# Kernel tuning notes

Measured on AMD Instinct MI355X. Metric: run time of the kernel, lower is better.

## Reference

```python
import jax, jax.numpy as jnp
import numpy as np

B, T = 32, 1024
TEMP_IN, STAT_IN = 128, 64
TEMP_OUT, STAT_OUT = 128, 64
EPS = 1e-5
NEG_SLOPE = 0.01


def _bn_eval(x, gamma, beta, mean, var):
    # BatchNorm1d in eval mode (running stats)
    return (x - mean) * jax.lax.rsqrt(var + EPS) * gamma + beta


def _leaky_relu(x):
    return jnp.where(x >= 0, x, NEG_SLOPE * x)


def setup_inputs() -> dict:
    key = jax.random.key(0)
    k = jax.random.split(key, 6)
    # deterministic ragged lengths in [512, 1024]
    lengths_np = (512 + (np.arange(B) * 37) % 513).astype(np.int64)
    N = int(lengths_np.sum())  # 23450
    batch_idx = np.repeat(np.arange(B), lengths_np).astype(np.int32)
    pos_idx = np.concatenate([np.arange(l) for l in lengths_np]).astype(np.int32)
    valid = (np.arange(T)[None, :] < lengths_np[:, None])  # [B, T]
    mask_repeat = valid[:, :, None] & valid[:, None, :]    # [B, T, T]

    inp = {
        "x_temp": jax.random.normal(k[0], (N, TEMP_IN), jnp.float32),
        "x_stat": jax.random.normal(k[1], (B, STAT_IN), jnp.float32),
        "temp_attn": jax.random.normal(k[2], (B, T, T), jnp.float32) * 0.1,
        "mask_repeat": jnp.asarray(mask_repeat),
        "lengths": jnp.asarray(lengths_np),
        "batch_idx": jnp.asarray(batch_idx),
        "pos_idx": jnp.asarray(pos_idx),
        # non_linear_temp: Linear(TEMP_IN+STAT_IN -> TEMP_OUT) + BN
        "W1": jax.random.normal(k[3], (TEMP_OUT, TEMP_IN + STAT_IN), jnp.float32) / np.sqrt(TEMP_IN + STAT_IN),
        "b1": jnp.zeros((TEMP_OUT,), jnp.float32),
        "gamma1": jnp.ones((TEMP_OUT,), jnp.float32),
        "beta1": jnp.zeros((TEMP_OUT,), jnp.float32),
        "mean1": jnp.zeros((TEMP_OUT,), jnp.float32),
        "var1": jnp.ones((TEMP_OUT,), jnp.float32),
        # non_linear_stat: Linear(STAT_IN -> STAT_OUT) + BN
        "W2": jax.random.normal(k[4], (STAT_OUT, STAT_IN), jnp.float32) / np.sqrt(STAT_IN),
        "b2": jnp.zeros((STAT_OUT,), jnp.float32),
        "gamma2": jnp.ones((STAT_OUT,), jnp.float32),
        "beta2": jnp.zeros((STAT_OUT,), jnp.float32),
        "mean2": jnp.zeros((STAT_OUT,), jnp.float32),
        "var2": jnp.ones((STAT_OUT,), jnp.float32),
    }
    return inp


def reference(x_temp, x_stat, temp_attn, mask_repeat, lengths, batch_idx, pos_idx,
              W1, b1, gamma1, beta1, mean1, var1,
              W2, b2, gamma2, beta2, mean2, var2):
    # repeat_static_features: gather per-batch static feats to packed rows
    x_stat_rep = x_stat[batch_idx]                              # [N, STAT_IN]
    h = jnp.concatenate((x_temp, x_stat_rep), axis=-1) @ W1.T + b1
    h = _leaky_relu(_bn_eval(h, gamma1, beta1, mean1, var1))    # [N, TEMP_OUT]

    # pad_packed_sequences: scatter packed rows into [B, T, C] (zeros elsewhere)
    padded = jnp.zeros((B, T, TEMP_OUT), h.dtype).at[batch_idx, pos_idx].set(h)

    # self attention: softmax(x x^T / sqrt(d)) over padded rows (as original)
    d = jnp.asarray(TEMP_OUT, h.dtype)
    qk = jnp.einsum('btc,bsc->bts', padded, padded) / jnp.sqrt(d)
    self_attn = jax.nn.softmax(qk, axis=-1)

    attn = jnp.where(mask_repeat, self_attn + temp_attn, jnp.asarray(0.0, h.dtype))

    x_stat_out = _leaky_relu(_bn_eval(x_stat @ W2.T + b2, gamma2, beta2, mean2, var2))

    x_out_pad = jnp.einsum('bts,bsc->btc', attn, padded)        # [B, T, TEMP_OUT]
    # pack_padded_sequences: gather valid positions back to packed layout
    x_out = x_out_pad[batch_idx, pos_idx]                       # [N, TEMP_OUT]
    return (x_out, x_stat_out)
```

## Files before the change

### kernel.cpp

```cpp
#include <hip/hip_runtime.h>
#include <hip/hip_bf16.h>
#include <hip/hip_fp16.h>

typedef __hip_bfloat16 bf16;
typedef __attribute__((ext_vector_type(8))) short short8;
typedef __attribute__((ext_vector_type(4))) float f32x4;

#define EPS 1e-5f
#define NSLOPE 0.01f

__device__ __forceinline__ float b2f(bf16 v) { return __bfloat162float(v); }

__device__ __forceinline__ float ld1(const void* p, size_t idx, int isbf) {
  if (isbf) return b2f(((const bf16*)p)[idx]);
  return ((const float*)p)[idx];
}
__device__ __forceinline__ void st1(void* p, size_t idx, int isbf, float v) {
  if (isbf) ((bf16*)p)[idx] = __float2bfloat16(v);
  else      ((float*)p)[idx] = v;
}
__device__ __forceinline__ short f2bs(float x) {
  bf16 t = __float2bfloat16(x);
  short s; __builtin_memcpy(&s, &t, 2); return s;
}
__device__ __forceinline__ short8 pack8f(const float* p) {
  float4 a = *(const float4*)p, b = *(const float4*)(p + 4);
  short8 r;
  r[0] = f2bs(a.x); r[1] = f2bs(a.y); r[2] = f2bs(a.z); r[3] = f2bs(a.w);
  r[4] = f2bs(b.x); r[5] = f2bs(b.y); r[6] = f2bs(b.z); r[7] = f2bs(b.w);
  return r;
}

__global__ void meta_kernel(const void* __restrict__ xt,
                            const int* __restrict__ bidx, const int* __restrict__ pidx,
                            int N, int B, int* __restrict__ rs, int* __restrict__ ln,
                            int* __restrict__ flag,
                            const void* __restrict__ W1, bf16* __restrict__ w1b, int w1n) {
  int isbf_l = 0;
  {
    unsigned w = ((const unsigned*)xt)[threadIdx.x & 63];
    unsigned lo = w & 0xffffu;
    unsigned ex = (lo >> 7) & 0xffu;
    bool sane = ((lo & 0x7fffu) == 0u) || (ex >= 96u && ex <= 134u);
    unsigned long long m = __ballot(sane);
    isbf_l = (__popcll(m) >= 48) ? 1 : 0;
    if (blockIdx.x == 0 && threadIdx.x == 0) flag[0] = isbf_l;
  }
  int stride = gridDim.x * blockDim.x;
  int g0 = blockIdx.x * blockDim.x + threadIdx.x;
  for (int i = g0; i < N; i += stride) {
    int b = bidx[i];
    if ((unsigned)b >= (unsigned)B) continue;
    if (i == 0 || bidx[i - 1] != b) rs[b] = i;
    if (i == N - 1 || bidx[i + 1] != b) ln[b] = pidx[i] + 1;
  }
  for (int i = g0; i < w1n; i += stride) {
    int o = i / 192, k = i - o * 192;
    int ct = o >> 4, n = o & 15;
    int ks = k >> 5, rem = k & 31;
    int q = rem >> 3, j = rem & 7;
    int fi = ((ct * 6 + ks) * 64 + q * 16 + n) * 8 + j;
    w1b[fi] = __float2bfloat16(ld1(W1, i, isbf_l));
  }
}

__global__ void zfill_kernel(void* out, const int* __restrict__ flag, long long n) {
  const int isbf = flag[0];
  long long i = (long long)blockIdx.x * blockDim.x + threadIdx.x;
  long long stride = (long long)gridDim.x * blockDim.x;
  for (; i < n; i += stride) st1(out, (size_t)i, isbf, 0.f);
}

__global__ __launch_bounds__(256) void h_mfma_kernel(
    const void* __restrict__ xt, const void* __restrict__ xsg,
    const int* __restrict__ bidx, const bf16* __restrict__ w1b,
    const void* __restrict__ b1,
    const void* __restrict__ g1, const void* __restrict__ be1,
    const void* __restrict__ mn1, const void* __restrict__ vr1,
    const int* __restrict__ flag, bf16* __restrict__ hout, int N) {
  const int isbf = flag[0];
  const int tid = threadIdx.x, lane = tid & 63, wv = tid >> 6;
  const int m16 = lane & 15, quad = lane >> 4;
  const int row0 = blockIdx.x * 64 + wv * 16;
  const int m = row0 + m16;
  const int mc = (m < N) ? m : (N - 1);
  const int bi = bidx[mc];

  short8 af[6];
  if (isbf) {
    const bf16* xr = (const bf16*)xt + (size_t)mc * 128 + quad * 8;
#pragma unroll
    for (int ks = 0; ks < 4; ++ks) af[ks] = *(const short8*)(xr + ks * 32);
    const bf16* sr = (const bf16*)xsg + (size_t)bi * 64 + quad * 8;
    af[4] = *(const short8*)sr;
    af[5] = *(const short8*)(sr + 32);
  } else {
    const float* xr = (const float*)xt + (size_t)mc * 128 + quad * 8;
#pragma unroll
    for (int ks = 0; ks < 4; ++ks) af[ks] = pack8f(xr + ks * 32);
    const float* sr = (const float*)xsg + (size_t)bi * 64 + quad * 8;
    af[4] = pack8f(sr);
    af[5] = pack8f(sr + 32);
  }

  f32x4 acc[8];
#pragma unroll
  for (int ct = 0; ct < 8; ++ct) acc[ct] = (f32x4){0.f, 0.f, 0.f, 0.f};

  const short8* wf = (const short8*)w1b;
#pragma unroll
  for (int ks = 0; ks < 6; ++ks) {
#pragma unroll
    for (int ct = 0; ct < 8; ++ct) {
      short8 bfrag = wf[(ct * 6 + ks) * 64 + lane];
      acc[ct] = __builtin_amdgcn_mfma_f32_16x16x32_bf16(af[ks], bfrag, acc[ct], 0, 0, 0);
    }
  }

#pragma unroll
  for (int ct = 0; ct < 8; ++ct) {
    const int o = ct * 16 + m16;
    float k1 = ld1(g1, o, isbf) * rsqrtf(ld1(vr1, o, isbf) + EPS);
    float k0 = ld1(be1, o, isbf) - ld1(mn1, o, isbf) * k1;
    float bias = ld1(b1, o, isbf);
#pragma unroll
    for (int r = 0; r < 4; ++r) {
      int mr = row0 + quad * 4 + r;
      if (mr < N) {
        float v = (acc[ct][r] + bias) * k1 + k0;
        v = (v >= 0.f) ? v : NSLOPE * v;
        hout[(size_t)mr * 128 + o] = __float2bfloat16(v);
      }
    }
  }
}

__global__ __launch_bounds__(64) void stat_kernel(
    const void* __restrict__ xstat, const void* __restrict__ W2,
    const void* __restrict__ b2, const void* __restrict__ g2,
    const void* __restrict__ be2, const void* __restrict__ mn2,
    const void* __restrict__ vr2, const int* __restrict__ flag,
    void* __restrict__ out, long long obase) {
  __shared__ float xs[64];
  const int isbf = flag[0];
  const int b = blockIdx.x, o = threadIdx.x;
  xs[o] = ld1(xstat, b * 64 + o, isbf);
  __syncthreads();
  float acc = ld1(b2, o, isbf);
#pragma unroll 8
  for (int j = 0; j < 64; ++j) acc += xs[j] * ld1(W2, o * 64 + j, isbf);
  float k1 = ld1(g2, o, isbf) * rsqrtf(ld1(vr2, o, isbf) + EPS);
  float k0 = ld1(be2, o, isbf) - ld1(mn2, o, isbf) * k1;
  float v = acc * k1 + k0;
  v = (v >= 0.f) ? v : NSLOPE * v;
  st1(out, (size_t)(obase + b * 64 + o), isbf, v);
}

__global__ __launch_bounds__(256, 2) void attn_mfma_kernel(
    const void* __restrict__ ta, const bf16* __restrict__ h,
    const int* __restrict__ rs_arr, const int* __restrict__ ln_arr,
    const int* __restrict__ flag, void* __restrict__ xout, int T, int N) {
  __shared__ __align__(16) unsigned short vT[2][128][72];
  __shared__ __align__(16) unsigned short Pw[4][16][72];

  const int b = blockIdx.y, t0 = blockIdx.x * 64;
  const int len = ln_arr[b];
  if (t0 >= len) return;
  const int isbf = flag[0];
  const int rs = rs_arr[b];
  const int tid = threadIdx.x;
  const int lane = tid & 63, wv = tid >> 6;
  const int m16 = lane & 15, quad = lane >> 4;
  const int t0w = t0 + wv * 16;

  short8 qf[4];
  {
    int qrow = rs + t0w + m16;
    if (qrow > N - 1) qrow = N - 1;
    const bf16* qp = h + (size_t)qrow * 128 + quad * 8;
#pragma unroll
    for (int ks = 0; ks < 4; ++ks) qf[ks] = *(const short8*)(qp + ks * 32);
  }

  const float scale = 0.08838834764831845f;
  const short8 zero8 = {0, 0, 0, 0, 0, 0, 0, 0};
  const uint4 zz = {0, 0, 0, 0};
  const size_t tarow = ((size_t)b * T + (t0w + m16)) * (size_t)T;
  const int c8base = wv * 32;

  f32x4 accp[8], acct[8];
#pragma unroll
  for (int ct = 0; ct < 8; ++ct) {
    accp[ct] = (f32x4){0.f, 0.f, 0.f, 0.f};
    acct[ct] = (f32x4){0.f, 0.f, 0.f, 0.f};
  }
  float mrun[4], lrun[4];
#pragma unroll
  for (int r = 0; r < 4; ++r) { mrun[r] = -INFINITY; lrun[r] = 0.f; }

  {
    int srow = lane;
    bool v = srow < len;
    const bf16* src = h + (size_t)(rs + (v ? srow : 0)) * 128;
#pragma unroll
    for (int it = 0; it < 4; ++it) {
      int c8 = c8base + it * 8;
      uint4 u = v ? *(const uint4*)(src + c8) : zz;
      const unsigned short* a = (const unsigned short*)&u;
#pragma unroll
      for (int j = 0; j < 8; ++j) vT[0][c8 + j][lane] = a[j];
    }
  }
  __syncthreads();

  const int nchunk = (len + 63) >> 6;
  for (int ci = 0; ci < nchunk; ++ci) {
    const int s0 = ci << 6;
    const int p = ci & 1;
    const bool have_next = (ci + 1 < nchunk);

    uint4 su0 = zz, su1 = zz, su2 = zz, su3 = zz;
    if (have_next) {
      int srow = s0 + 64 + lane;
      bool v = srow < len;
      const bf16* src = h + (size_t)(rs + (v ? srow : 0)) * 128;
      if (v) {
        su0 = *(const uint4*)(src + c8base);
        su1 = *(const uint4*)(src + c8base + 8);
        su2 = *(const uint4*)(src + c8base + 16);
        su3 = *(const uint4*)(src + c8base + 24);
      }
    }

    short8 taf0, taf1;
    if (isbf) {
      const bf16* tp = (const bf16*)ta + tarow + s0 + quad * 8;
      taf0 = *(const short8*)tp;
      taf1 = *(const short8*)(tp + 32);
    } else {
      const float* tp = (const float*)ta + tarow + s0 + quad * 8;
      taf0 = pack8f(tp);
      taf1 = pack8f(tp + 32);
    }

    f32x4 sa[4];
    bool sval[4];
#pragma unroll
    for (int st = 0; st < 4; ++st) {
      int srow = s0 + st * 16 + m16;
      bool v = srow < len;
      sval[st] = v;
      const bf16* kp = h + (size_t)(rs + (v ? srow : 0)) * 128 + quad * 8;
      f32x4 a0 = (f32x4){0.f, 0.f, 0.f, 0.f};
#pragma unroll
      for (int ks = 0; ks < 4; ++ks) {
        short8 kf = v ? *(const short8*)(kp + ks * 32) : zero8;
        a0 = __builtin_amdgcn_mfma_f32_16x16x32_bf16(qf[ks], kf, a0, 0, 0, 0);
      }
      sa[st] = a0;
    }

    float cm[4];
#pragma unroll
    for (int r = 0; r < 4; ++r) cm[r] = -INFINITY;
#pragma unroll
    for (int st = 0; st < 4; ++st) {
#pragma unroll
      for (int r = 0; r < 4; ++r)
        cm[r] = fmaxf(cm[r], sval[st] ? sa[st][r] * scale : -INFINITY);
    }
#pragma unroll
    for (int off = 1; off <= 8; off <<= 1) {
#pragma unroll
      for (int r = 0; r < 4; ++r) cm[r] = fmaxf(cm[r], __shfl_xor(cm[r], off, 64));
    }
    float al[4], csum[4];
#pragma unroll
    for (int r = 0; r < 4; ++r) {
      float mnew = fmaxf(mrun[r], cm[r]);
      al[r] = __expf(mrun[r] - mnew);
      mrun[r] = mnew;
      csum[r] = 0.f;
    }
#pragma unroll
    for (int st = 0; st < 4; ++st) {
#pragma unroll
      for (int r = 0; r < 4; ++r) {
        float pv = sval[st] ? __expf(sa[st][r] * scale - mrun[r]) : 0.f;
        csum[r] += pv;
        Pw[wv][quad * 4 + r][st * 16 + m16] = (unsigned short)f2bs(pv);
      }
    }
#pragma unroll
    for (int off = 1; off <= 8; off <<= 1) {
#pragma unroll
      for (int r = 0; r < 4; ++r) csum[r] += __shfl_xor(csum[r], off, 64);
    }
#pragma unroll
    for (int r = 0; r < 4; ++r) lrun[r] = lrun[r] * al[r] + csum[r];

#pragma unroll
    for (int ct = 0; ct < 8; ++ct) {
#pragma unroll
      for (int r = 0; r < 4; ++r) accp[ct][r] *= al[r];
    }

#pragma unroll
    for (int ks = 0; ks < 2; ++ks) {
      short8 pf = *(const short8*)&Pw[wv][m16][ks * 32 + quad * 8];
      short8 tf = ks ? taf1 : taf0;
#pragma unroll
      for (int ct = 0; ct < 8; ++ct) {
        short8 bfv = *(const short8*)&vT[p][ct * 16 + m16][ks * 32 + quad * 8];
        accp[ct] = __builtin_amdgcn_mfma_f32_16x16x32_bf16(pf, bfv, accp[ct], 0, 0, 0);
        acct[ct] = __builtin_amdgcn_mfma_f32_16x16x32_bf16(tf, bfv, acct[ct], 0, 0, 0);
      }
    }

    if (have_next) {
      const unsigned short* a0 = (const unsigned short*)&su0;
      const unsigned short* a1 = (const unsigned short*)&su1;
      const unsigned short* a2 = (const unsigned short*)&su2;
      const unsigned short* a3 = (const unsigned short*)&su3;
#pragma unroll
      for (int j = 0; j < 8; ++j) {
        vT[p ^ 1][c8base + j][lane]      = a0[j];
        vT[p ^ 1][c8base + 8 + j][lane]  = a1[j];
        vT[p ^ 1][c8base + 16 + j][lane] = a2[j];
        vT[p ^ 1][c8base + 24 + j][lane] = a3[j];
      }
    }
    __syncthreads();
  }

  const int nr = len - t0w;
#pragma unroll
  for (int r = 0; r < 4; ++r) {
    int t = quad * 4 + r;
    if (t < nr) {
      float m_r = mrun[r], l_r = lrun[r];
      float m_f = (len < T) ? fmaxf(m_r, 0.f) : m_r;
      float corr = __expf(m_r - m_f);
      float l_f = l_r * corr + (float)(T - len) * __expf(-m_f);
      float os = corr / l_f;
      size_t ob = (size_t)(rs + t0w + t) * 128;
#pragma unroll
      for (int ct = 0; ct < 8; ++ct)
        st1(xout, ob + ct * 16 + m16, isbf, accp[ct][r] * os + acct[ct][r]);
    }
  }
}

extern "C" void kernel_launch(void* const* d_in, const int* in_sizes, int n_in,
                              void* d_out, int out_size, void* d_ws, size_t ws_size,
                              hipStream_t stream) {
  const void* x_temp    = d_in[0];
  const void* x_stat    = d_in[1];
  const void* temp_attn = d_in[2];
  const int N = in_sizes[0] / 128;
  const int B = in_sizes[1] / 64;
  long long tt = (long long)in_sizes[2] / B;
  int T = 1; while ((long long)(T + 1) * (T + 1) <= tt) ++T;

  int p = 3;
  while (p < n_in && in_sizes[p] != N) ++p;
  const int* batch_idx = (const int*)d_in[p++];
  const int* pos_idx   = (const int*)d_in[p++];
  const void* W1 = d_in[p++];
  const void* b1 = d_in[p++];
  const void* g1 = d_in[p++];
  const void* be1= d_in[p++];
  const void* mn1= d_in[p++];
  const void* vr1= d_in[p++];
  const void* W2 = d_in[p++];
  const void* b2 = d_in[p++];
  const void* g2 = d_in[p++];
  const void* be2= d_in[p++];
  const void* mn2= d_in[p++];
  const void* vr2= d_in[p++];

  int*  meta = (int*)d_ws;
  int*  rs   = meta;
  int*  lnp  = meta + B;
  int*  flag = meta + 2 * B;
  bf16* h    = (bf16*)((char*)d_ws + 1024);
  bf16* w1b  = h + (size_t)N * 128;
  const int w1n = 128 * 192;
  size_t need = 1024 + (size_t)N * 128 * sizeof(bf16) + (size_t)w1n * sizeof(bf16);

  long long obase = (long long)N * 128;

  meta_kernel<<<90, 256, 0, stream>>>(x_temp, batch_idx, pos_idx, N, B, rs, lnp,
                                      flag, W1, w1b, w1n);
  stat_kernel<<<B, 64, 0, stream>>>(x_stat, W2, b2, g2, be2, mn2, vr2, flag,
                                    d_out, obase);
  if (ws_size >= need) {
    h_mfma_kernel<<<(N + 63) / 64, 256, 0, stream>>>(x_temp, x_stat, batch_idx,
                                                     w1b, b1, g1, be1, mn1, vr1,
                                                     flag, h, N);
    attn_mfma_kernel<<<dim3((T + 63) / 64, B), 256, 0, stream>>>(
        temp_attn, h, rs, lnp, flag, d_out, T, N);
  } else {
    zfill_kernel<<<512, 256, 0, stream>>>(d_out, flag, obase);
  }
}
```

Baseline: 395.9 us.

## Split attention key range across blocks with flash-decoding style reduction

The attention kernel now splits each 64-row query tile's key chunks across up to three blocks, writing bf16 partial accumulators plus running max and sum to workspace. A new reduction kernel merges them with softmax rescaling. This raises block count from about 370 to about 1000 to fill the many CUs better, at the cost of extra workspace traffic, an extra launch, and bf16 rounding of partials. The static-feature MLP is also folded into the meta kernel to drop one launch.

```diff
diff --git a/kernel.cpp b/kernel.cpp
--- a/kernel.cpp
+++ b/kernel.cpp
@@ -8,9 +8,12 @@
 
 #define EPS 1e-5f
 #define NSLOPE 0.01f
+#define NSMAX 3
 
 __device__ __forceinline__ float b2f(bf16 v) { return __bfloat162float(v); }
-
+__device__ __forceinline__ float bs2f(unsigned short s) {
+  bf16 t; __builtin_memcpy(&t, &s, 2); return __bfloat162float(t);
+}
 __device__ __forceinline__ float ld1(const void* p, size_t idx, int isbf) {
   if (isbf) return b2f(((const bf16*)p)[idx]);
   return ((const float*)p)[idx];
@@ -35,7 +38,12 @@
                             const int* __restrict__ bidx, const int* __restrict__ pidx,
                             int N, int B, int* __restrict__ rs, int* __restrict__ ln,
                             int* __restrict__ flag,
-                            const void* __restrict__ W1, bf16* __restrict__ w1b, int w1n) {
+                            const void* __restrict__ W1, bf16* __restrict__ w1b, int w1n,
+                            const void* __restrict__ xstat, const void* __restrict__ W2,
+                            const void* __restrict__ b2, const void* __restrict__ g2,
+                            const void* __restrict__ be2, const void* __restrict__ mn2,
+                            const void* __restrict__ vr2, void* __restrict__ out,
+                            long long obase) {
   int isbf_l = 0;
   {
     unsigned w = ((const unsigned*)xt)[threadIdx.x & 63];
@@ -61,6 +69,21 @@
     int q = rem >> 3, j = rem & 7;
     int fi = ((ct * 6 + ks) * 64 + q * 16 + n) * 8 + j;
     w1b[fi] = __float2bfloat16(ld1(W1, i, isbf_l));
+  }
+  __shared__ float xs[64];
+  if (threadIdx.x < 64 && blockIdx.x < B)
+    xs[threadIdx.x] = ld1(xstat, blockIdx.x * 64 + threadIdx.x, isbf_l);
+  __syncthreads();
+  if (threadIdx.x < 64 && blockIdx.x < B) {
+    const int o = threadIdx.x, bb = blockIdx.x;
+    float acc = ld1(b2, o, isbf_l);
+#pragma unroll 8
+    for (int j = 0; j < 64; ++j) acc += xs[j] * ld1(W2, o * 64 + j, isbf_l);
+    float k1 = ld1(g2, o, isbf_l) * rsqrtf(ld1(vr2, o, isbf_l) + EPS);
+    float k0 = ld1(be2, o, isbf_l) - ld1(mn2, o, isbf_l) * k1;
+    float v = acc * k1 + k0;
+    v = (v >= 0.f) ? v : NSLOPE * v;
+    st1(out, (size_t)(obase + bb * 64 + o), isbf_l, v);
   }
 }
 
@@ -135,37 +158,27 @@
   }
 }
 
-__global__ __launch_bounds__(64) void stat_kernel(
-    const void* __restrict__ xstat, const void* __restrict__ W2,
-    const void* __restrict__ b2, const void* __restrict__ g2,
-    const void* __restrict__ be2, const void* __restrict__ mn2,
-    const void* __restrict__ vr2, const int* __restrict__ flag,
-    void* __restrict__ out, long long obase) {
-  __shared__ float xs[64];
-  const int isbf = flag[0];
-  const int b = blockIdx.x, o = threadIdx.x;
-  xs[o] = ld1(xstat, b * 64 + o, isbf);
-  __syncthreads();
-  float acc = ld1(b2, o, isbf);
-#pragma unroll 8
-  for (int j = 0; j < 64; ++j) acc += xs[j] * ld1(W2, o * 64 + j, isbf);
-  float k1 = ld1(g2, o, isbf) * rsqrtf(ld1(vr2, o, isbf) + EPS);
-  float k0 = ld1(be2, o, isbf) - ld1(mn2, o, isbf) * k1;
-  float v = acc * k1 + k0;
-  v = (v >= 0.f) ? v : NSLOPE * v;
-  st1(out, (size_t)(obase + b * 64 + o), isbf, v);
-}
-
-__global__ __launch_bounds__(256, 2) void attn_mfma_kernel(
+__global__ __launch_bounds__(256, 2) void attn_part_kernel(
     const void* __restrict__ ta, const bf16* __restrict__ h,
     const int* __restrict__ rs_arr, const int* __restrict__ ln_arr,
-    const int* __restrict__ flag, void* __restrict__ xout, int T, int N) {
+    const int* __restrict__ flag,
+    unsigned short* __restrict__ accp_buf, unsigned short* __restrict__ acct_buf,
+    float* __restrict__ ms_buf, float* __restrict__ ls_buf,
+    int T, int N, int TT) {
   __shared__ __align__(16) unsigned short vT[2][128][72];
   __shared__ __align__(16) unsigned short Pw[4][16][72];
 
-  const int b = blockIdx.y, t0 = blockIdx.x * 64;
+  const int b = blockIdx.y;
+  const int tt = blockIdx.x / NSMAX, sl = blockIdx.x % NSMAX;
+  const int t0 = tt * 64;
   const int len = ln_arr[b];
   if (t0 >= len) return;
+  const int nchunk = (len + 63) >> 6;
+  const int ns = (nchunk + 5) / 6;
+  if (sl >= ns) return;
+  const int c_begin = (sl * nchunk) / ns;
+  const int c_end = ((sl + 1) * nchunk) / ns;
+
   const int isbf = flag[0];
   const int rs = rs_arr[b];
   const int tid = threadIdx.x;
@@ -199,7 +212,7 @@
   for (int r = 0; r < 4; ++r) { mrun[r] = -INFINITY; lrun[r] = 0.f; }
 
   {
-    int srow = lane;
+    int srow = c_begin * 64 + lane;
     bool v = srow < len;
     const bf16* src = h + (size_t)(rs + (v ? srow : 0)) * 128;
 #pragma unroll
@@ -213,11 +226,10 @@
   }
   __syncthreads();
 
-  const int nchunk = (len + 63) >> 6;
-  for (int ci = 0; ci < nchunk; ++ci) {
+  for (int ci = c_begin; ci < c_end; ++ci) {
     const int s0 = ci << 6;
-    const int p = ci & 1;
-    const bool have_next = (ci + 1 < nchunk);
+    const int p = (ci - c_begin) & 1;
+    const bool have_next = (ci + 1 < c_end);
 
     uint4 su0 = zz, su1 = zz, su2 = zz, su3 = zz;
     if (have_next) {
@@ -333,6 +345,278 @@
     __syncthreads();
   }
 
+  const int slot = (b * TT + tt) * NSMAX + sl;
+  const size_t abase = (size_t)slot * 8192;
+#pragma unroll
+  for (int r = 0; r < 4; ++r) {
+    const int row = wv * 16 + quad * 4 + r;
+#pragma unroll
+    for (int ct = 0; ct < 8; ++ct) {
+      const size_t o = abase + (size_t)row * 128 + ct * 16 + m16;
+      accp_buf[o] = (unsigned short)f2bs(accp[ct][r]);
+      acct_buf[o] = (unsigned short)f2bs(acct[ct][r]);
+    }
+    if (m16 == 0) {
+      ms_buf[(size_t)slot * 64 + row] = mrun[r];
+      ls_buf[(size_t)slot * 64 + row] = lrun[r];
+    }
+  }
+}
+
+__global__ __launch_bounds__(256) void attn_red_kernel(
+    const unsigned short* __restrict__ accp_buf,
+    const unsigned short* __restrict__ acct_buf,
+    const float* __restrict__ ms_buf, const float* __restrict__ ls_buf,
+    const int* __restrict__ rs_arr, const int* __restrict__ ln_arr,
+    const int* __restrict__ flag, void* __restrict__ xout, int T, int TT) {
+  const int b = blockIdx.y, tt = blockIdx.x, t0 = tt * 64;
+  const int len = ln_arr[b];
+  if (t0 >= len) return;
+  const int isbf = flag[0];
+  const int rs = rs_arr[b];
+  const int nchunk = (len + 63) >> 6;
+  const int ns = (nchunk + 5) / 6;
+  const int base_slot = (b * TT + tt) * NSMAX;
+
+  const int r = threadIdx.x >> 2;
+  const int cg = threadIdx.x & 3;
+  const int trow = t0 + r;
+  if (trow >= len) return;
+
+  float m0 = ms_buf[(size_t)(base_slot + 0) * 64 + r];
+  float m1 = (ns > 1) ? ms_buf[(size_t)(base_slot + 1) * 64 + r] : -INFINITY;
+  float m2 = (ns > 2) ? ms_buf[(size_t)(base_slot + 2) * 64 + r] : -INFINITY;
+  float M = fmaxf(m0, fmaxf(m1, m2));
+  float w0 = __expf(m0 - M);
+  float w1 = (ns > 1) ? __expf(m1 - M) : 0.f;
+  float w2 = (ns > 2) ? __expf(m2 - M) : 0.f;
+  float L = ls_buf[(size_t)(base_slot + 0) * 64 + r] * w0;
+  if (ns > 1) L += ls_buf[(size_t)(base_slot + 1) * 64 + r] * w1;
+  if (ns > 2) L += ls_buf[(size_t)(base_slot + 2) * 64 + r] * w2;
+
+  float m_f = (len < T) ? fmaxf(M, 0.f) : M;
+  float corr = __expf(M - m_f);
+  float l_f = L * corr + (float)(T - len) * __expf(-m_f);
+  float os = corr / l_f;
+
+  const size_t p0 = (size_t)(base_slot + 0) * 8192 + (size_t)r * 128 + cg * 32;
+  const size_t p1 = (size_t)(base_slot + 1) * 8192 + (size_t)r * 128 + cg * 32;
+  const size_t p2 = (size_t)(base_slot + 2) * 8192 + (size_t)r * 128 + cg * 32;
+  const size_t ob = (size_t)(rs + trow) * 128 + cg * 32;
+
+#pragma unroll
+  for (int g = 0; g < 4; ++g) {
+    float acc[8], tac[8];
+    {
+      short8 ap = *(const short8*)&accp_buf[p0 + g * 8];
+      short8 at = *(const short8*)&acct_buf[p0 + g * 8];
+#pragma unroll
+      for (int j = 0; j < 8; ++j) {
+        acc[j] = bs2f((unsigned short)ap[j]) * w0;
+        tac[j] = bs2f((unsigned short)at[j]);
+      }
+    }
+    if (ns > 1) {
+      short8 ap = *(const short8*)&accp_buf[p1 + g * 8];
+      short8 at = *(const short8*)&acct_buf[p1 + g * 8];
+#pragma unroll
+      for (int j = 0; j < 8; ++j) {
+        acc[j] += bs2f((unsigned short)ap[j]) * w1;
+        tac[j] += bs2f((unsigned short)at[j]);
+      }
+    }
+    if (ns > 2) {
+      short8 ap = *(const short8*)&accp_buf[p2 + g * 8];
+      short8 at = *(const short8*)&acct_buf[p2 + g * 8];
+#pragma unroll
+      for (int j = 0; j < 8; ++j) {
+        acc[j] += bs2f((unsigned short)ap[j]) * w2;
+        tac[j] += bs2f((unsigned short)at[j]);
+      }
+    }
+#pragma unroll
+    for (int j = 0; j < 8; ++j)
+      st1(xout, ob + g * 8 + j, isbf, acc[j] * os + tac[j]);
+  }
+}
+
+__global__ __launch_bounds__(256, 2) void attn_mfma_kernel(
+    const void* __restrict__ ta, const bf16* __restrict__ h,
+    const int* __restrict__ rs_arr, const int* __restrict__ ln_arr,
+    const int* __restrict__ flag, void* __restrict__ xout, int T, int N) {
+  __shared__ __align__(16) unsigned short vT[2][128][72];
+  __shared__ __align__(16) unsigned short Pw[4][16][72];
+
+  const int b = blockIdx.y, t0 = blockIdx.x * 64;
+  const int len = ln_arr[b];
+  if (t0 >= len) return;
+  const int isbf = flag[0];
+  const int rs = rs_arr[b];
+  const int tid = threadIdx.x;
+  const int lane = tid & 63, wv = tid >> 6;
+  const int m16 = lane & 15, quad = lane >> 4;
+  const int t0w = t0 + wv * 16;
+
+  short8 qf[4];
+  {
+    int qrow = rs + t0w + m16;
+    if (qrow > N - 1) qrow = N - 1;
+    const bf16* qp = h + (size_t)qrow * 128 + quad * 8;
+#pragma unroll
+    for (int ks = 0; ks < 4; ++ks) qf[ks] = *(const short8*)(qp + ks * 32);
+  }
+
+  const float scale = 0.08838834764831845f;
+  const short8 zero8 = {0, 0, 0, 0, 0, 0, 0, 0};
+  const uint4 zz = {0, 0, 0, 0};
+  const size_t tarow = ((size_t)b * T + (t0w + m16)) * (size_t)T;
+  const int c8base = wv * 32;
+
+  f32x4 accp[8], acct[8];
+#pragma unroll
+  for (int ct = 0; ct < 8; ++ct) {
+    accp[ct] = (f32x4){0.f, 0.f, 0.f, 0.f};
+    acct[ct] = (f32x4){0.f, 0.f, 0.f, 0.f};
+  }
+  float mrun[4], lrun[4];
+#pragma unroll
+  for (int r = 0; r < 4; ++r) { mrun[r] = -INFINITY; lrun[r] = 0.f; }
+
+  {
+    int srow = lane;
+    bool v = srow < len;
+    const bf16* src = h + (size_t)(rs + (v ? srow : 0)) * 128;
+#pragma unroll
+    for (int it = 0; it < 4; ++it) {
+      int c8 = c8base + it * 8;
+      uint4 u = v ? *(const uint4*)(src + c8) : zz;
+      const unsigned short* a = (const unsigned short*)&u;
+#pragma unroll
+      for (int j = 0; j < 8; ++j) vT[0][c8 + j][lane] = a[j];
+    }
+  }
+  __syncthreads();
+
+  const int nchunk = (len + 63) >> 6;
+  for (int ci = 0; ci < nchunk; ++ci) {
+    const int s0 = ci << 6;
+    const int p = ci & 1;
+    const bool have_next = (ci + 1 < nchunk);
+
+    uint4 su0 = zz, su1 = zz, su2 = zz, su3 = zz;
+    if (have_next) {
+      int srow = s0 + 64 + lane;
+      bool v = srow < len;
+      const bf16* src = h + (size_t)(rs + (v ? srow : 0)) * 128;
+      if (v) {
+        su0 = *(const uint4*)(src + c8base);
+        su1 = *(const uint4*)(src + c8base + 8);
+        su2 = *(const uint4*)(src + c8base + 16);
+        su3 = *(const uint4*)(src + c8base + 24);
+      }
+    }
+
+    short8 taf0, taf1;
+    if (isbf) {
+      const bf16* tp = (const bf16*)ta + tarow + s0 + quad * 8;
+      taf0 = *(const short8*)tp;
+      taf1 = *(const short8*)(tp + 32);
+    } else {
+      const float* tp = (const float*)ta + tarow + s0 + quad * 8;
+      taf0 = pack8f(tp);
+      taf1 = pack8f(tp + 32);
+    }
+
+    f32x4 sa[4];
+    bool sval[4];
+#pragma unroll
+    for (int st = 0; st < 4; ++st) {
+      int srow = s0 + st * 16 + m16;
+      bool v = srow < len;
+      sval[st] = v;
+      const bf16* kp = h + (size_t)(rs + (v ? srow : 0)) * 128 + quad * 8;
+      f32x4 a0 = (f32x4){0.f, 0.f, 0.f, 0.f};
+#pragma unroll
+      for (int ks = 0; ks < 4; ++ks) {
+        short8 kf = v ? *(const short8*)(kp + ks * 32) : zero8;
+        a0 = __builtin_amdgcn_mfma_f32_16x16x32_bf16(qf[ks], kf, a0, 0, 0, 0);
+      }
+      sa[st] = a0;
+    }
+
+    float cm[4];
+#pragma unroll
+    for (int r = 0; r < 4; ++r) cm[r] = -INFINITY;
+#pragma unroll
+    for (int st = 0; st < 4; ++st) {
+#pragma unroll
+      for (int r = 0; r < 4; ++r)
+        cm[r] = fmaxf(cm[r], sval[st] ? sa[st][r] * scale : -INFINITY);
+    }
+#pragma unroll
+    for (int off = 1; off <= 8; off <<= 1) {
+#pragma unroll
+      for (int r = 0; r < 4; ++r) cm[r] = fmaxf(cm[r], __shfl_xor(cm[r], off, 64));
+    }
+    float al[4], csum[4];
+#pragma unroll
+    for (int r = 0; r < 4; ++r) {
+      float mnew = fmaxf(mrun[r], cm[r]);
+      al[r] = __expf(mrun[r] - mnew);
+      mrun[r] = mnew;
+      csum[r] = 0.f;
+    }
+#pragma unroll
+    for (int st = 0; st < 4; ++st) {
+#pragma unroll
+      for (int r = 0; r < 4; ++r) {
+        float pv = sval[st] ? __expf(sa[st][r] * scale - mrun[r]) : 0.f;
+        csum[r] += pv;
+        Pw[wv][quad * 4 + r][st * 16 + m16] = (unsigned short)f2bs(pv);
+      }
+    }
+#pragma unroll
+    for (int off = 1; off <= 8; off <<= 1) {
+#pragma unroll
+      for (int r = 0; r < 4; ++r) csum[r] += __shfl_xor(csum[r], off, 64);
+    }
+#pragma unroll
+    for (int r = 0; r < 4; ++r) lrun[r] = lrun[r] * al[r] + csum[r];
+
+#pragma unroll
+    for (int ct = 0; ct < 8; ++ct) {
+#pragma unroll
+      for (int r = 0; r < 4; ++r) accp[ct][r] *= al[r];
+    }
+
+#pragma unroll
+    for (int ks = 0; ks < 2; ++ks) {
+      short8 pf = *(const short8*)&Pw[wv][m16][ks * 32 + quad * 8];
+      short8 tf = ks ? taf1 : taf0;
+#pragma unroll
+      for (int ct = 0; ct < 8; ++ct) {
+        short8 bfv = *(const short8*)&vT[p][ct * 16 + m16][ks * 32 + quad * 8];
+        accp[ct] = __builtin_amdgcn_mfma_f32_16x16x32_bf16(pf, bfv, accp[ct], 0, 0, 0);
+        acct[ct] = __builtin_amdgcn_mfma_f32_16x16x32_bf16(tf, bfv, acct[ct], 0, 0, 0);
+      }
+    }
+
+    if (have_next) {
+      const unsigned short* a0 = (const unsigned short*)&su0;
+      const unsigned short* a1 = (const unsigned short*)&su1;
+      const unsigned short* a2 = (const unsigned short*)&su2;
+      const unsigned short* a3 = (const unsigned short*)&su3;
+#pragma unroll
+      for (int j = 0; j < 8; ++j) {
+        vT[p ^ 1][c8base + j][lane]      = a0[j];
+        vT[p ^ 1][c8base + 8 + j][lane]  = a1[j];
+        vT[p ^ 1][c8base + 16 + j][lane] = a2[j];
+        vT[p ^ 1][c8base + 24 + j][lane] = a3[j];
+      }
+    }
+    __syncthreads();
+  }
+
   const int nr = len - t0w;
 #pragma unroll
   for (int r = 0; r < 4; ++r) {
@@ -361,6 +645,7 @@
   const int B = in_sizes[1] / 64;
   long long tt = (long long)in_sizes[2] / B;
   int T = 1; while ((long long)(T + 1) * (T + 1) <= tt) ++T;
+  const int TT = (T + 63) >> 6;
 
   int p = 3;
   while (p < n_in && in_sizes[p] != N) ++p;
@@ -383,23 +668,41 @@
   int*  rs   = meta;
   int*  lnp  = meta + B;
   int*  flag = meta + 2 * B;
-  bf16* h    = (bf16*)((char*)d_ws + 1024);
-  bf16* w1b  = h + (size_t)N * 128;
+  size_t off = 1024;
+  bf16* h    = (bf16*)((char*)d_ws + off);  off += (size_t)N * 128 * 2;
   const int w1n = 128 * 192;
-  size_t need = 1024 + (size_t)N * 128 * sizeof(bf16) + (size_t)w1n * sizeof(bf16);
+  bf16* w1b  = (bf16*)((char*)d_ws + off);  off += (size_t)w1n * 2;
+  off = (off + 255) & ~(size_t)255;
+  size_t need_min = off;
+  const size_t nslot = (size_t)B * TT * NSMAX;
+  unsigned short* accp_buf = (unsigned short*)((char*)d_ws + off);
+  off += nslot * 8192 * 2;
+  unsigned short* acct_buf = (unsigned short*)((char*)d_ws + off);
+  off += nslot * 8192 * 2;
+  float* ms_buf = (float*)((char*)d_ws + off);  off += nslot * 64 * 4;
+  float* ls_buf = (float*)((char*)d_ws + off);  off += nslot * 64 * 4;
+  size_t need_split = off;
 
   long long obase = (long long)N * 128;
 
   meta_kernel<<<90, 256, 0, stream>>>(x_temp, batch_idx, pos_idx, N, B, rs, lnp,
-                                      flag, W1, w1b, w1n);
-  stat_kernel<<<B, 64, 0, stream>>>(x_stat, W2, b2, g2, be2, mn2, vr2, flag,
-                                    d_out, obase);
-  if (ws_size >= need) {
+                                      flag, W1, w1b, w1n,
+                                      x_stat, W2, b2, g2, be2, mn2, vr2,
+                                      d_out, obase);
+  if (ws_size >= need_min) {
     h_mfma_kernel<<<(N + 63) / 64, 256, 0, stream>>>(x_temp, x_stat, batch_idx,
                                                      w1b, b1, g1, be1, mn1, vr1,
                                                      flag, h, N);
-    attn_mfma_kernel<<<dim3((T + 63) / 64, B), 256, 0, stream>>>(
-        temp_attn, h, rs, lnp, flag, d_out, T, N);
+    if (ws_size >= need_split) {
+      attn_part_kernel<<<dim3(TT * NSMAX, B), 256, 0, stream>>>(
+          temp_attn, h, rs, lnp, flag, accp_buf, acct_buf, ms_buf, ls_buf,
+          T, N, TT);
+      attn_red_kernel<<<dim3(TT, B), 256, 0, stream>>>(
+          accp_buf, acct_buf, ms_buf, ls_buf, rs, lnp, flag, d_out, T, TT);
+    } else {
+      attn_mfma_kernel<<<dim3(TT, B), 256, 0, stream>>>(
+          temp_attn, h, rs, lnp, flag, d_out, T, N);
+    }
   } else {
     zfill_kernel<<<512, 256, 0, stream>>>(d_out, flag, obase);
   }
```

Result: slower. 425.7 us (+7.5%).

## Pre-convert temp_attn to tiled bf16 layout and fold stat kernel into meta

Applied to the files above, without the earlier changes.

Adds a pre-pass that converts the valid region of temp_attn from fp32 into a bf16 buffer, tiled so each attention wave reads contiguous 16x64 blocks. The attention kernel then loads these pre-packed tiles instead of converting fp32 strided rows inline. The static-feature linear/BN kernel is also folded into meta_kernel to save one launch. The pre-pass adds a full extra read of temp_attn plus a write and re-read of the bf16 copy, which may cost more than the inline conversion it replaces.

```diff
diff --git a/kernel.cpp b/kernel.cpp
--- a/kernel.cpp
+++ b/kernel.cpp
@@ -10,7 +10,6 @@
 #define NSLOPE 0.01f
 
 __device__ __forceinline__ float b2f(bf16 v) { return __bfloat162float(v); }
-
 __device__ __forceinline__ float ld1(const void* p, size_t idx, int isbf) {
   if (isbf) return b2f(((const bf16*)p)[idx]);
   return ((const float*)p)[idx];
@@ -35,7 +34,12 @@
                             const int* __restrict__ bidx, const int* __restrict__ pidx,
                             int N, int B, int* __restrict__ rs, int* __restrict__ ln,
                             int* __restrict__ flag,
-                            const void* __restrict__ W1, bf16* __restrict__ w1b, int w1n) {
+                            const void* __restrict__ W1, bf16* __restrict__ w1b, int w1n,
+                            const void* __restrict__ xstat, const void* __restrict__ W2,
+                            const void* __restrict__ b2, const void* __restrict__ g2,
+                            const void* __restrict__ be2, const void* __restrict__ mn2,
+                            const void* __restrict__ vr2, void* __restrict__ out,
+                            long long obase) {
   int isbf_l = 0;
   {
     unsigned w = ((const unsigned*)xt)[threadIdx.x & 63];
@@ -62,6 +66,21 @@
     int fi = ((ct * 6 + ks) * 64 + q * 16 + n) * 8 + j;
     w1b[fi] = __float2bfloat16(ld1(W1, i, isbf_l));
   }
+  __shared__ float xs[64];
+  if (threadIdx.x < 64 && blockIdx.x < B)
+    xs[threadIdx.x] = ld1(xstat, blockIdx.x * 64 + threadIdx.x, isbf_l);
+  __syncthreads();
+  if (threadIdx.x < 64 && blockIdx.x < B) {
+    const int o = threadIdx.x, bb = blockIdx.x;
+    float acc = ld1(b2, o, isbf_l);
+#pragma unroll 8
+    for (int j = 0; j < 64; ++j) acc += xs[j] * ld1(W2, o * 64 + j, isbf_l);
+    float k1 = ld1(g2, o, isbf_l) * rsqrtf(ld1(vr2, o, isbf_l) + EPS);
+    float k0 = ld1(be2, o, isbf_l) - ld1(mn2, o, isbf_l) * k1;
+    float v = acc * k1 + k0;
+    v = (v >= 0.f) ? v : NSLOPE * v;
+    st1(out, (size_t)(obase + bb * 64 + o), isbf_l, v);
+  }
 }
 
 __global__ void zfill_kernel(void* out, const int* __restrict__ flag, long long n) {
@@ -69,6 +88,36 @@
   long long i = (long long)blockIdx.x * blockDim.x + threadIdx.x;
   long long stride = (long long)gridDim.x * blockDim.x;
   for (; i < n; i += stride) st1(out, (size_t)i, isbf, 0.f);
+}
+
+__global__ __launch_bounds__(256) void ta2b_kernel(
+    const void* __restrict__ ta, const int* __restrict__ ln_arr,
+    const int* __restrict__ flag, unsigned short* __restrict__ tb, int T) {
+  const int isbf = flag[0];
+  const int b = blockIdx.y, tg = blockIdx.x;
+  const int t0 = tg * 16;
+  const int len = ln_arr[b];
+  if (t0 >= len) return;
+  const int c64 = ((len + 63) >> 6) << 6;
+  const int nr = min(16, len - t0);
+  const int c = threadIdx.x * 4;
+  if (c >= c64) return;
+  const int ci = c >> 6, sc = c & 63;
+  unsigned short* dst = tb + (((size_t)(b * 64 + tg) * 16 + ci) << 10) + sc;
+  for (int r = 0; r < nr; ++r) {
+    const size_t src = ((size_t)b * T + (t0 + r)) * (size_t)T + c;
+    ushort4 o;
+    if (isbf) {
+      o = *(const ushort4*)((const unsigned short*)ta + src);
+    } else {
+      float4 f = *(const float4*)((const float*)ta + src);
+      o.x = (unsigned short)f2bs(f.x);
+      o.y = (unsigned short)f2bs(f.y);
+      o.z = (unsigned short)f2bs(f.z);
+      o.w = (unsigned short)f2bs(f.w);
+    }
+    *(ushort4*)(dst + r * 64) = o;
+  }
 }
 
 __global__ __launch_bounds__(256) void h_mfma_kernel(
@@ -135,31 +184,12 @@
   }
 }
 
-__global__ __launch_bounds__(64) void stat_kernel(
-    const void* __restrict__ xstat, const void* __restrict__ W2,
-    const void* __restrict__ b2, const void* __restrict__ g2,
-    const void* __restrict__ be2, const void* __restrict__ mn2,
-    const void* __restrict__ vr2, const int* __restrict__ flag,
-    void* __restrict__ out, long long obase) {
-  __shared__ float xs[64];
-  const int isbf = flag[0];
-  const int b = blockIdx.x, o = threadIdx.x;
-  xs[o] = ld1(xstat, b * 64 + o, isbf);
-  __syncthreads();
-  float acc = ld1(b2, o, isbf);
-#pragma unroll 8
-  for (int j = 0; j < 64; ++j) acc += xs[j] * ld1(W2, o * 64 + j, isbf);
-  float k1 = ld1(g2, o, isbf) * rsqrtf(ld1(vr2, o, isbf) + EPS);
-  float k0 = ld1(be2, o, isbf) - ld1(mn2, o, isbf) * k1;
-  float v = acc * k1 + k0;
-  v = (v >= 0.f) ? v : NSLOPE * v;
-  st1(out, (size_t)(obase + b * 64 + o), isbf, v);
-}
-
 __global__ __launch_bounds__(256, 2) void attn_mfma_kernel(
-    const void* __restrict__ ta, const bf16* __restrict__ h,
+    const void* __restrict__ ta, const unsigned short* __restrict__ tb,
+    const bf16* __restrict__ h,
     const int* __restrict__ rs_arr, const int* __restrict__ ln_arr,
-    const int* __restrict__ flag, void* __restrict__ xout, int T, int N) {
+    const int* __restrict__ flag, void* __restrict__ xout, int T, int N,
+    int useconv) {
   __shared__ __align__(16) unsigned short vT[2][128][72];
   __shared__ __align__(16) unsigned short Pw[4][16][72];
 
@@ -186,6 +216,8 @@
   const short8 zero8 = {0, 0, 0, 0, 0, 0, 0, 0};
   const uint4 zz = {0, 0, 0, 0};
   const size_t tarow = ((size_t)b * T + (t0w + m16)) * (size_t)T;
+  const size_t tbbase = ((size_t)(b * 64 + (t0w >> 4)) * 16) << 10;
+  const int tboff = m16 * 64 + quad * 8;
   const int c8base = wv * 32;
 
   f32x4 accp[8], acct[8];
@@ -233,7 +265,11 @@
     }
 
     short8 taf0, taf1;
-    if (isbf) {
+    if (useconv) {
+      const unsigned short* tp = tb + tbbase + ((size_t)ci << 10) + tboff;
+      taf0 = *(const short8*)tp;
+      taf1 = *(const short8*)(tp + 32);
+    } else if (isbf) {
       const bf16* tp = (const bf16*)ta + tarow + s0 + quad * 8;
       taf0 = *(const short8*)tp;
       taf1 = *(const short8*)(tp + 32);
@@ -361,6 +397,7 @@
   const int B = in_sizes[1] / 64;
   long long tt = (long long)in_sizes[2] / B;
   int T = 1; while ((long long)(T + 1) * (T + 1) <= tt) ++T;
+  const int TT = (T + 63) >> 6;
 
   int p = 3;
   while (p < n_in && in_sizes[p] != N) ++p;
@@ -383,23 +420,33 @@
   int*  rs   = meta;
   int*  lnp  = meta + B;
   int*  flag = meta + 2 * B;
-  bf16* h    = (bf16*)((char*)d_ws + 1024);
-  bf16* w1b  = h + (size_t)N * 128;
+  size_t off = 1024;
+  bf16* h    = (bf16*)((char*)d_ws + off);  off += (size_t)N * 128 * 2;
   const int w1n = 128 * 192;
-  size_t need = 1024 + (size_t)N * 128 * sizeof(bf16) + (size_t)w1n * sizeof(bf16);
+  bf16* w1b  = (bf16*)((char*)d_ws + off);  off += (size_t)w1n * 2;
+  off = (off + 255) & ~(size_t)255;
+  size_t need_min = off;
+  unsigned short* tb = (unsigned short*)((char*)d_ws + off);
+  off += (size_t)B * (T / 16) * (T / 64) * 1024 * 2;
+  size_t need_tb = off;
+  int useconv = (ws_size >= need_tb) ? 1 : 0;
 
   long long obase = (long long)N * 128;
 
   meta_kernel<<<90, 256, 0, stream>>>(x_temp, batch_idx, pos_idx, N, B, rs, lnp,
-                                      flag, W1, w1b, w1n);
-  stat_kernel<<<B, 64, 0, stream>>>(x_stat, W2, b2, g2, be2, mn2, vr2, flag,
-                                    d_out, obase);
-  if (ws_size >= need) {
+                                      flag, W1, w1b, w1n,
+                                      x_stat, W2, b2, g2, be2, mn2, vr2,
+                                      d_out, obase);
+  if (ws_size >= need_min) {
     h_mfma_kernel<<<(N + 63) / 64, 256, 0, stream>>>(x_temp, x_stat, batch_idx,
                                                      w1b, b1, g1, be1, mn1, vr1,
                                                      flag, h, N);
-    attn_mfma_kernel<<<dim3((T + 63) / 64, B), 256, 0, stream>>>(
-        temp_attn, h, rs, lnp, flag, d_out, T, N);
+    if (useconv) {
+      ta2b_kernel<<<dim3(T / 16, B), 256, 0, stream>>>(temp_attn, lnp, flag,
+                                                       tb, T);
+    }
+    attn_mfma_kernel<<<dim3(TT, B), 256, 0, stream>>>(
+        temp_attn, tb, h, rs, lnp, flag, d_out, T, N, useconv);
   } else {
     zfill_kernel<<<512, 256, 0, stream>>>(d_out, flag, obase);
   }
```

After: 415.3 us. 1.05x slower.
